# Kernel tuning notes

Measured on AMD Instinct MI355X. Metric: run time of the kernel, lower is better.

## Reference

```python
import jax, jax.numpy as jnp
import numpy as np

N = 100000       # nodes
D_IN = 256       # input feature dim
HID = 128        # hidden dim (GCN output)
D_OUT = 64       # SGCL output dim
NNZ = 1600000    # nnz of gcn adjacency
E = 500000       # directed edges (adj_e)
BIE = 1000000    # bidirectional edges (adj_n)


def setup_inputs() -> dict:
    key = jax.random.key(0)
    ks = jax.random.split(key, 13)
    X = jax.random.normal(ks[0], (N, D_IN), jnp.float32)
    # weight scales chosen so exp(logstd) stays well-conditioned (glorot-like)
    W_gcn = jax.random.normal(ks[1], (D_IN, HID), jnp.float32) * 0.05
    W_miu = jax.random.normal(ks[2], (2 * HID, D_OUT), jnp.float32) * 0.01
    W_sigma = jax.random.normal(ks[3], (2 * HID, D_OUT), jnp.float32) * 0.01
    gcn_values = jax.random.uniform(ks[4], (NNZ,), jnp.float32)
    bi_values = jax.random.uniform(ks[5], (BIE,), jnp.float32)
    noise_in = jax.random.normal(ks[6], (E, D_OUT), jnp.float32)
    noise_out = jax.random.normal(ks[7], (E, D_OUT), jnp.float32)
    noise_node = jax.random.normal(ks[8], (N, D_OUT), jnp.float32)
    gcn_indices = jax.random.randint(ks[9], (2, NNZ), 0, N)
    di_edges = jax.random.randint(ks[10], (2, E), 0, N)
    # ensure every node has at least one incident bi-edge (source side) so that
    # log(aggregated variance) is finite, as with a real symmetric adjacency
    bi_src = jnp.concatenate([jnp.arange(N), jax.random.randint(ks[11], (BIE - N,), 0, N)])
    bi_dst = jax.random.randint(ks[12], (BIE,), 0, N)
    bi_edges = jnp.stack([bi_src, bi_dst], axis=0)
    return {
        "X": X, "W_gcn": W_gcn, "W_miu": W_miu, "W_sigma": W_sigma,
        "gcn_values": gcn_values, "bi_values": bi_values,
        "noise_in": noise_in, "noise_out": noise_out, "noise_node": noise_node,
        "gcn_indices": gcn_indices, "di_edges": di_edges, "bi_edges": bi_edges,
    }


def reference(X, W_gcn, W_miu, W_sigma, gcn_values, bi_values,
              noise_in, noise_out, noise_node, gcn_indices, di_edges, bi_edges):
    n = X.shape[0]
    hid = W_gcn.shape[1]
    # ---- GraphConvSparse with identity activation: adj @ (X @ W) ----
    xw = X @ W_gcn                                     # [N, HID]
    msgs = gcn_values[:, None] * xw[gcn_indices[1]]    # [NNZ, HID]
    hidden = jax.ops.segment_sum(msgs, gcn_indices[0], num_segments=n)
    # split weights: concat([h_a, h_b]) @ W == h_a @ W_top + h_b @ W_bot
    Wm_t, Wm_b = W_miu[:hid], W_miu[hid:]
    Ws_t, Ws_b = W_sigma[:hid], W_sigma[hid:]
    # ---- edge embedding (directed edges) ----
    h_src = hidden[di_edges[0]]                        # [E, HID]
    h_dst = hidden[di_edges[1]]                        # [E, HID]
    miu_in = h_src @ Wm_t + h_dst @ Wm_b               # [E, D_OUT]
    miu_out = h_dst @ Wm_t + h_src @ Wm_b
    logstd_in = h_src @ Ws_t + h_dst @ Ws_b
    logstd_out = h_dst @ Ws_t + h_src @ Ws_b
    edge_in = noise_in * jnp.exp(logstd_in) + miu_in
    edge_out = noise_out * jnp.exp(logstd_out) + miu_out
    # ---- node embedding (bidirectional edges, weighted scatter-aggregate) ----
    b0 = hidden[bi_edges[0]]                           # [BIE, HID]
    b1 = hidden[bi_edges[1]]
    bi_miu = b0 @ Wm_t + b1 @ Wm_b                     # [BIE, D_OUT]
    bi_logstd = b0 @ Ws_t + b1 @ Ws_b
    node_miu = jax.ops.segment_sum(bi_values[:, None] * bi_miu, bi_edges[0], num_segments=n)
    node_var = jax.ops.segment_sum((bi_values ** 2)[:, None] * jnp.exp(bi_logstd), bi_edges[0], num_segments=n)
    node_logstd = 0.5 * jnp.log(node_var)
    node_embed = noise_node * jnp.exp(node_logstd) + node_miu
    return (node_embed, edge_in, edge_out)
```

## Files before the change

### kernel.cpp

```cpp
#include <hip/hip_runtime.h>

typedef unsigned short u16t;
typedef unsigned int   u32t;
typedef unsigned long long u64t;

#define NNODE 100000
#define DIN   256
#define HIDN  128
#define DOUTN 64
#define NNZE  1600000
#define EDIR  500000
#define EBI   1000000
#define G64   1563
#define NBIN  782
#define CH3   4096
#define K3G   391
#define K3B   245
#define CAPG  2432
#define CAPB  1536
#define EBLK  15625

typedef __attribute__((ext_vector_type(8))) short bf16x8;
typedef __attribute__((ext_vector_type(4))) float f32x4;
typedef __attribute__((ext_vector_type(4))) float f4v;

__device__ __forceinline__ u16t f2bf(float f){
  u32t u = __float_as_uint(f);
  u += 0x7FFFu + ((u>>16)&1u);
  return (u16t)(u>>16);
}
__device__ __forceinline__ float2 up2(u32t w){
  return make_float2(__uint_as_float(w<<16), __uint_as_float(w&0xFFFF0000u));
}

__global__ __launch_bounds__(256) void prep_kernel(const float* __restrict__ Wg,
                                                   const float* __restrict__ Wm,
                                                   const float* __restrict__ Wsg,
                                                   u16t* __restrict__ Wg_pre,
                                                   u16t* __restrict__ Wc_pre){
  int idx = blockIdx.x*256 + threadIdx.x;
  int e = idx & 7, l = (idx>>3) & 63, f = (idx>>9) & 63, sel = idx>>15;
  int k_in = ((e>>2)<<4) + ((l>>4)<<2) + (e&3);
  if(sel == 0){
    int ks = f>>3, nf = f&7;
    int k = ks*32 + k_in, n = nf*16 + (l&15);
    Wg_pre[idx] = f2bf(Wg[(size_t)k*HIDN + n]);
  } else {
    int ks = f>>4, nf = f&15;
    int k = ks*32 + k_in, c = nf*16 + (l&15);
    int half = c>>7, ci = c&127;
    const float* src = (ci&1) ? Wsg : Wm;
    Wc_pre[idx - 32768] = f2bf(src[(size_t)(half*128 + k)*DOUTN + (ci>>1)]);
  }
}

__global__ __launch_bounds__(256) void coarse_hist_kernel(const int* __restrict__ gi,
                                                          const int* __restrict__ be,
                                                          u32t* __restrict__ gcnt_c,
                                                          u32t* __restrict__ bcnt_c){
  __shared__ u32t h[1024];
  int blk = blockIdx.x, t = threadIdx.x;
  const int* keys; u32t* outc; int E, e0;
  if(blk < K3G){ keys=gi; outc=gcnt_c; E=NNZE; e0=blk*CH3; }
  else         { keys=be; outc=bcnt_c; E=EBI;  e0=(blk-K3G)*CH3; }
  for(int i=t;i<1024;i+=256) h[i]=0;
  __syncthreads();
  for(int i=t;i<CH3;i+=256){
    int e=e0+i;
    if(e<E) atomicAdd(&h[(u32t)keys[e]>>7], 1u);
  }
  __syncthreads();
  for(int b=t;b<1024;b+=256){
    u32t c=h[b];
    if(c) atomicAdd(&outc[b], c);
  }
}

__global__ __launch_bounds__(256) void scan_coarse_kernel(u32t* __restrict__ gcnt_c,
                                                          u32t* __restrict__ gcoff,
                                                          u32t* __restrict__ gcur_,
                                                          u32t* __restrict__ bcnt_c,
                                                          u32t* __restrict__ bcoff,
                                                          u32t* __restrict__ bcur_){
  __shared__ u32t part[256];
  u32t *cnt, *coff, *cur;
  if(blockIdx.x==0){ cnt=gcnt_c; coff=gcoff; cur=gcur_; }
  else             { cnt=bcnt_c; coff=bcoff; cur=bcur_; }
  int t = threadIdx.x;
  u32t ch[4], s=0;
  #pragma unroll
  for(int j=0;j<4;j++){ int idx=t*4+j; ch[j] = (idx<NBIN)? cnt[idx] : 0u; s+=ch[j]; }
  part[t]=s; __syncthreads();
  for(int off=1;off<256;off<<=1){
    u32t x=(t>=off)?part[t-off]:0u;
    __syncthreads();
    part[t]+=x;
    __syncthreads();
  }
  u32t run=(t==0)?0u:part[t-1];
  #pragma unroll
  for(int j=0;j<4;j++){
    int idx=t*4+j;
    if(idx<NBIN){ coff[idx]=run; cur[idx]=run; run+=ch[j]; }
  }
  if(t==255) coff[NBIN]=part[255];
}

__global__ __launch_bounds__(256) void part_kernel(const int* __restrict__ gi,
                                                   const float* __restrict__ gv,
                                                   const int* __restrict__ be,
                                                   const float* __restrict__ bv,
                                                   u32t* __restrict__ gcur_,
                                                   u64t* __restrict__ gbuck,
                                                   u32t* __restrict__ bcur_,
                                                   u64t* __restrict__ bbuck){
  __shared__ u32t hist[1024];
  __shared__ u32t scn[1024];
  __shared__ u32t part[256];
  __shared__ u32t base[1024];
  __shared__ u64t ebuf[CH3];
  __shared__ u16t binsArr[CH3];
  int blk = blockIdx.x, t = threadIdx.x;
  const int *keys, *pay; const float* val; u32t* cursor; u64t* buck; int E, e0;
  if(blk < K3G){ keys=gi; pay=gi+NNZE; val=gv; cursor=gcur_; buck=gbuck; E=NNZE; e0=blk*CH3; }
  else         { keys=be; pay=be+EBI;  val=bv; cursor=bcur_; buck=bbuck; E=EBI;  e0=(blk-K3G)*CH3; }
  for(int i=t;i<1024;i+=256) hist[i]=0;
  __syncthreads();
  for(int i=t;i<CH3;i+=256){
    int e=e0+i;
    if(e<E) atomicAdd(&hist[(u32t)keys[e]>>7], 1u);
  }
  __syncthreads();
  u32t ch[4], s=0;
  #pragma unroll
  for(int j=0;j<4;j++){ ch[j]=hist[t*4+j]; s+=ch[j]; }
  part[t]=s; __syncthreads();
  for(int off=1;off<256;off<<=1){
    u32t x=(t>=off)?part[t-off]:0u;
    __syncthreads();
    part[t]+=x;
    __syncthreads();
  }
  u32t run=(t==0)?0u:part[t-1];
  #pragma unroll
  for(int j=0;j<4;j++){ scn[t*4+j]=run; run+=ch[j]; }
  __syncthreads();
  for(int i=t;i<1024;i+=256) hist[i]=scn[i];
  __syncthreads();
  for(int i=t;i<CH3;i+=256){
    int e=e0+i;
    if(e<E){
      int k = keys[e];
      u32t b = (u32t)k>>7;
      u32t p = atomicAdd(&hist[b],1u);
      u64t ent = (u64t)((u32t)pay[e] | (((u32t)k&127u)<<20)) | ((u64t)__float_as_uint(val[e])<<32);
      ebuf[p]=ent; binsArr[p]=(u16t)b;
    }
  }
  __syncthreads();
  for(int b=t;b<1024;b+=256){
    u32t c = hist[b]-scn[b];
    base[b] = c ? atomicAdd(&cursor[b], c) : 0u;
  }
  __syncthreads();
  int totalValid = part[255];
  for(int i=t;i<totalValid;i+=256){
    u32t b = binsArr[i];
    buck[ (size_t)base[b] + (u32t)i - scn[b] ] = ebuf[i];
  }
}

__global__ __launch_bounds__(256) void gemm1_kernel(const float* __restrict__ X,
                                                    const u16t* __restrict__ Wg_pre,
                                                    u16t* __restrict__ xwb){
  __shared__ __align__(16) u16t Xs[64*256];
  const int t = threadIdx.x, l = t & 63, w = t >> 6;
  const int row0 = blockIdx.x * 64;
  for(int i=0;i<16;i++){
    int m = w*16 + i;
    int mg = min(row0 + m, NNODE-1);
    f4v f = __builtin_nontemporal_load((const f4v*)&X[(size_t)mg*DIN + l*4]);
    u32t lo = (u32t)f2bf(f[0]) | ((u32t)f2bf(f[1])<<16);
    u32t hi = (u32t)f2bf(f[2]) | ((u32t)f2bf(f[3])<<16);
    u32t* p = (u32t*)&Xs[m*256 + ((l ^ (m&15))<<2)];
    p[0] = lo; p[1] = hi;
  }
  __syncthreads();
  f32x4 acc[8];
  #pragma unroll
  for(int nf=0;nf<8;nf++) acc[nf] = (f32x4)(0.f);
  const int lm = l & 15, l4 = l >> 4;
  const int mrow = w*16 + lm;
  #pragma unroll 1
  for(int ks=0; ks<8; ks++){
    int kg = ks*8 + l4;
    union { uint2 u2[2]; bf16x8 v; } a;
    a.u2[0] = *(const uint2*)&Xs[mrow*256 + ((kg     ^ lm)<<2)];
    a.u2[1] = *(const uint2*)&Xs[mrow*256 + (((kg+4) ^ lm)<<2)];
    #pragma unroll
    for(int nf=0;nf<8;nf++){
      union { uint4 u4; bf16x8 v; } b;
      b.u4 = *(const uint4*)&Wg_pre[(size_t)((ks*8+nf)*64 + l)*8];
      acc[nf] = __builtin_amdgcn_mfma_f32_16x16x32_bf16(a.v, b.v, acc[nf], 0, 0, 0);
    }
  }
  #pragma unroll
  for(int r=0;r<4;r++){
    int gr = row0 + w*16 + l4*4 + r;
    if(gr < NNODE){
      #pragma unroll
      for(int nf=0;nf<8;nf++)
        xwb[(size_t)gr*HIDN + nf*16 + lm] = f2bf(acc[nf][r]);
    }
  }
}

__global__ __launch_bounds__(256) void gcn_gather2_kernel(const u16t* __restrict__ xwb,
                                                          const u64t* __restrict__ gbuck,
                                                          const u32t* __restrict__ gcoff,
                                                          u32t* __restrict__ hiddenw){
  __shared__ u64t ebuf[CAPG];
  __shared__ u32t hist[128], offs[129], cur[128], sc[128];
  int bin = blockIdx.x, t = threadIdx.x;
  u32t base = gcoff[bin], cnt = gcoff[bin+1] - base;
  if(t<128) hist[t]=0;
  __syncthreads();
  for(u32t i=t;i<cnt;i+=256)
    atomicAdd(&hist[(u32t)(gbuck[base+i]>>20)&127u], 1u);
  __syncthreads();
  if(t<128) sc[t]=hist[t];
  __syncthreads();
  for(int off=1;off<128;off<<=1){
    u32t x=(t>=off&&t<128)?sc[t-off]:0u;
    __syncthreads();
    if(t<128) sc[t]+=x;
    __syncthreads();
  }
  if(t<128){ offs[t+1]=sc[t]; cur[t]=sc[t]-hist[t]; if(t==0) offs[0]=0u; }
  __syncthreads();
  for(u32t i=t;i<cnt;i+=256){
    u64t e = gbuck[base+i];
    u32t p = atomicAdd(&cur[(u32t)(e>>20)&127u], 1u);
    ebuf[p]=e;
  }
  __syncthreads();
  int w=t>>6, l=t&63;
  const u32t* xww=(const u32t*)xwb;
  for(int idx=w; idx<128; idx+=4){
    int n = bin*128 + idx;
    if(n >= NNODE) continue;
    u32t s0=offs[idx], cnt2=offs[idx+1]-s0;
    float acc0=0.f, acc1=0.f;
    u32t nbr=(cnt2+3)&~3u;
    for(u32t j=0;j<nbr;j+=4){
      float2 xs[4]; float vs[4];
      #pragma unroll
      for(int q=0;q<4;q++){
        u32t jj=j+q;
        u64t e=(jj<cnt2)? ebuf[s0+jj] : 0ULL;
        vs[q]=__uint_as_float((u32t)(e>>32));
        xs[q]=up2(xww[(size_t)(e&0x1FFFFu)*64 + l]);
      }
      #pragma unroll
      for(int q=0;q<4;q++){ acc0+=vs[q]*xs[q].x; acc1+=vs[q]*xs[q].y; }
    }
    hiddenw[(size_t)n*64 + l] = (u32t)f2bf(acc0) | ((u32t)f2bf(acc1)<<16);
  }
}

__global__ __launch_bounds__(256) void gemm2_kernel(u32t* __restrict__ hiddenw,
                                                    const u16t* __restrict__ Wc_pre,
                                                    u16t* __restrict__ DSTw){
  __shared__ __align__(16) u16t Hs[64*128];
  const int t = threadIdx.x, l = t & 63, w = t >> 6;
  const int row0 = blockIdx.x * 64;
  for(int i=0;i<16;i++){
    int m = w*16 + i;
    int mg = min(row0 + m, NNODE-1);
    u32t v = hiddenw[(size_t)mg*64 + l];
    *(u32t*)&Hs[m*128 + (((l>>1) ^ (m&15))<<2) + ((l&1)<<1)] = v;
  }
  __syncthreads();
  f32x4 acc[16];
  #pragma unroll
  for(int nf=0;nf<16;nf++) acc[nf] = (f32x4)(0.f);
  const int lm = l & 15, l4 = l >> 4;
  const int mrow = w*16 + lm;
  #pragma unroll 1
  for(int ks=0; ks<4; ks++){
    int kg = ks*8 + l4;
    union { uint2 u2[2]; bf16x8 v; } a;
    a.u2[0] = *(const uint2*)&Hs[mrow*128 + ((kg     ^ lm)<<2)];
    a.u2[1] = *(const uint2*)&Hs[mrow*128 + (((kg+4) ^ lm)<<2)];
    #pragma unroll
    for(int nf=0;nf<16;nf++){
      union { uint4 u4; bf16x8 v; } b;
      b.u4 = *(const uint4*)&Wc_pre[(size_t)((ks*16+nf)*64 + l)*8];
      acc[nf] = __builtin_amdgcn_mfma_f32_16x16x32_bf16(a.v, b.v, acc[nf], 0, 0, 0);
    }
  }
  u16t* SRCw = (u16t*)hiddenw;
  #pragma unroll
  for(int r=0;r<4;r++){
    int gr = row0 + w*16 + l4*4 + r;
    if(gr < NNODE){
      #pragma unroll
      for(int nf=0;nf<8;nf++)
        SRCw[(size_t)gr*HIDN + nf*16 + lm] = f2bf(acc[nf][r]);
      #pragma unroll
      for(int nf=8;nf<16;nf++)
        DSTw[(size_t)gr*HIDN + (nf-8)*16 + lm] = f2bf(acc[nf][r]);
    }
  }
}

__global__ __launch_bounds__(256) void edgebi2_kernel(const u16t* __restrict__ SRCb,
                                                      const u16t* __restrict__ DSTb,
                                                      const int*  __restrict__ ed,
                                                      const float* __restrict__ nin,
                                                      const float* __restrict__ nout,
                                                      float* __restrict__ ein,
                                                      float* __restrict__ eout,
                                                      const u64t* __restrict__ bbuck,
                                                      const u32t* __restrict__ bcoff,
                                                      const float* __restrict__ nn,
                                                      float* __restrict__ outp){
  __shared__ u64t ebuf[CAPB];
  __shared__ u32t hist[128], offs[129], cur[128], sc[128];
  const int t = threadIdx.x;
  const u32t* Sw = (const u32t*)SRCb;
  const u32t* Dw = (const u32t*)DSTb;
  if(blockIdx.x >= NBIN){
    const int e0 = ((int)(blockIdx.x - NBIN)*4 + (t>>6))*8;
    const int l = t & 63;
    int s[8], d[8];
    #pragma unroll
    for(int q=0;q<8;q++){ s[q] = ed[e0+q]; d[q] = ed[EDIR+e0+q]; }
    float2 Ss[8], Ds[8], Sd[8], Dd[8];
    float ni[8], no[8];
    #pragma unroll
    for(int q=0;q<8;q++){
      Ss[q] = up2(Sw[(size_t)s[q]*64 + l]);
      Ds[q] = up2(Dw[(size_t)s[q]*64 + l]);
      Sd[q] = up2(Sw[(size_t)d[q]*64 + l]);
      Dd[q] = up2(Dw[(size_t)d[q]*64 + l]);
      ni[q] = __builtin_nontemporal_load(&nin[(size_t)(e0+q)*DOUTN + l]);
      no[q] = __builtin_nontemporal_load(&nout[(size_t)(e0+q)*DOUTN + l]);
    }
    #pragma unroll
    for(int q=0;q<8;q++){
      size_t o = (size_t)(e0+q)*DOUTN + l;
      float miu_in  = Ss[q].x + Dd[q].x, ls_in  = Ss[q].y + Dd[q].y;
      float miu_out = Sd[q].x + Ds[q].x, ls_out = Sd[q].y + Ds[q].y;
      __builtin_nontemporal_store(ni[q] * __expf(ls_in)  + miu_in,  &ein[o]);
      __builtin_nontemporal_store(no[q] * __expf(ls_out) + miu_out, &eout[o]);
    }
    return;
  }
  int bin = blockIdx.x;
  u32t base = bcoff[bin], cnt = bcoff[bin+1] - base;
  if(t<128) hist[t]=0;
  __syncthreads();
  for(u32t i=t;i<cnt;i+=256)
    atomicAdd(&hist[(u32t)(bbuck[base+i]>>20)&127u], 1u);
  __syncthreads();
  if(t<128) sc[t]=hist[t];
  __syncthreads();
  for(int off=1;off<128;off<<=1){
    u32t x=(t>=off&&t<128)?sc[t-off]:0u;
    __syncthreads();
    if(t<128) sc[t]+=x;
    __syncthreads();
  }
  if(t<128){ offs[t+1]=sc[t]; cur[t]=sc[t]-hist[t]; if(t==0) offs[0]=0u; }
  __syncthreads();
  for(u32t i=t;i<cnt;i+=256){
    u64t e = bbuck[base+i];
    u32t p = atomicAdd(&cur[(u32t)(e>>20)&127u], 1u);
    ebuf[p]=e;
  }
  __syncthreads();
  int w=t>>6, l=t&63;
  for(int idx=w; idx<128; idx+=4){
    int n = bin*128 + idx;
    if(n >= NNODE) continue;
    float2 S = up2(Sw[(size_t)n*64 + l]);
    u32t s0=offs[idx], cnt2=offs[idx+1]-s0;
    float nmiu=0.f, nvar=0.f;
    u32t nbr=(cnt2+3)&~3u;
    for(u32t j=0;j<nbr;j+=4){
      float2 Dq[4]; float vs[4];
      #pragma unroll
      for(int q=0;q<4;q++){
        u32t jj=j+q;
        u64t e=(jj<cnt2)? ebuf[s0+jj] : 0ULL;
        vs[q]=__uint_as_float((u32t)(e>>32));
        Dq[q]=up2(Dw[(size_t)(e&0x1FFFFu)*64 + l]);
      }
      #pragma unroll
      for(int q=0;q<4;q++){
        nmiu += vs[q]*(S.x+Dq[q].x);
        nvar += vs[q]*vs[q]*__expf(S.y+Dq[q].y);
      }
    }
    size_t o = (size_t)n*DOUTN + l;
    float nd = __builtin_nontemporal_load(&nn[o]);
    __builtin_nontemporal_store(nd*sqrtf(nvar) + nmiu, &outp[o]);
  }
}

extern "C" void kernel_launch(void* const* d_in, const int* in_sizes, int n_in,
                              void* d_out, int out_size, void* d_ws, size_t ws_size,
                              hipStream_t stream){
  const float* X    = (const float*)d_in[0];
  const float* Wg   = (const float*)d_in[1];
  const float* Wm   = (const float*)d_in[2];
  const float* Wsg  = (const float*)d_in[3];
  const float* gv   = (const float*)d_in[4];
  const float* bv   = (const float*)d_in[5];
  const float* nin  = (const float*)d_in[6];
  const float* nout = (const float*)d_in[7];
  const float* nnod = (const float*)d_in[8];
  const int*  gi   = (const int*)d_in[9];
  const int*  ed   = (const int*)d_in[10];
  const int*  be   = (const int*)d_in[11];

  char* ws = (char*)d_ws;
  u64t*  gbuck   = (u64t*)ws;
  u16t*  xwb     = (u16t*)(ws + 12800000);
  u32t*  gcnt_c  = (u32t*)(ws + 38400000);
  u32t*  bcnt_c  = (u32t*)(ws + 38404096);
  u32t*  gcoff   = (u32t*)(ws + 38408192);
  u32t*  gcur_   = (u32t*)(ws + 38412288);
  u32t*  bcoff   = (u32t*)(ws + 38416384);
  u32t*  bcur_   = (u32t*)(ws + 38420480);
  u64t*  bbuck   = (u64t*)(ws + 40003168);
  u32t*  hiddenw = (u32t*)(ws + 51200000);
  u16t*  SRCw    = (u16t*)hiddenw;
  u16t*  DSTw    = (u16t*)ws;

  float* out  = (float*)d_out;
  float* ein  = out + (size_t)NNODE*DOUTN;
  float* eout = ein + (size_t)EDIR*DOUTN;
  u16t* Wg_pre = (u16t*)((char*)d_out + 25600000 - 131072);
  u16t* Wc_pre = Wg_pre + 32768;

  (void)hipMemsetAsync(gcnt_c, 0, 8192, stream);
  coarse_hist_kernel<<<K3G+K3B, 256, 0, stream>>>(gi, be, gcnt_c, bcnt_c);
  scan_coarse_kernel<<<2,       256, 0, stream>>>(gcnt_c, gcoff, gcur_, bcnt_c, bcoff, bcur_);
  part_kernel       <<<K3G+K3B, 256, 0, stream>>>(gi, gv, be, bv, gcur_, gbuck, bcur_, bbuck);
  prep_kernel       <<<256,     256, 0, stream>>>(Wg, Wm, Wsg, Wg_pre, Wc_pre);
  gemm1_kernel      <<<G64,     256, 0, stream>>>(X, Wg_pre, xwb);
  gcn_gather2_kernel<<<NBIN,    256, 0, stream>>>(xwb, gbuck, gcoff, hiddenw);
  gemm2_kernel      <<<G64,     256, 0, stream>>>(hiddenw, Wc_pre, DSTw);
  edgebi2_kernel    <<<NBIN+EBLK, 256, 0, stream>>>(SRCw, DSTw, ed, nin, nout,
                                                    ein, eout, bbuck, bcoff, nnod, out);
}
```

Baseline: 446.7 us.

## Merge weight prep into histogram kernel and partition into gemm1 launch

```diff
diff --git a/kernel.cpp b/kernel.cpp
--- a/kernel.cpp
+++ b/kernel.cpp
@@ -16,6 +16,7 @@
 #define CH3   4096
 #define K3G   391
 #define K3B   245
+#define KPART (K3G+K3B)
 #define CAPG  2432
 #define CAPB  1536
 #define EBLK  15625
@@ -33,33 +34,34 @@
   return make_float2(__uint_as_float(w<<16), __uint_as_float(w&0xFFFF0000u));
 }
 
-__global__ __launch_bounds__(256) void prep_kernel(const float* __restrict__ Wg,
-                                                   const float* __restrict__ Wm,
-                                                   const float* __restrict__ Wsg,
-                                                   u16t* __restrict__ Wg_pre,
-                                                   u16t* __restrict__ Wc_pre){
-  int idx = blockIdx.x*256 + threadIdx.x;
-  int e = idx & 7, l = (idx>>3) & 63, f = (idx>>9) & 63, sel = idx>>15;
-  int k_in = ((e>>2)<<4) + ((l>>4)<<2) + (e&3);
-  if(sel == 0){
-    int ks = f>>3, nf = f&7;
-    int k = ks*32 + k_in, n = nf*16 + (l&15);
-    Wg_pre[idx] = f2bf(Wg[(size_t)k*HIDN + n]);
-  } else {
-    int ks = f>>4, nf = f&15;
-    int k = ks*32 + k_in, c = nf*16 + (l&15);
-    int half = c>>7, ci = c&127;
-    const float* src = (ci&1) ? Wsg : Wm;
-    Wc_pre[idx - 32768] = f2bf(src[(size_t)(half*128 + k)*DOUTN + (ci>>1)]);
-  }
-}
-
-__global__ __launch_bounds__(256) void coarse_hist_kernel(const int* __restrict__ gi,
-                                                          const int* __restrict__ be,
-                                                          u32t* __restrict__ gcnt_c,
-                                                          u32t* __restrict__ bcnt_c){
+__global__ __launch_bounds__(256) void histprep_kernel(const int* __restrict__ gi,
+                                                       const int* __restrict__ be,
+                                                       u32t* __restrict__ gcnt_c,
+                                                       u32t* __restrict__ bcnt_c,
+                                                       const float* __restrict__ Wg,
+                                                       const float* __restrict__ Wm,
+                                                       const float* __restrict__ Wsg,
+                                                       u16t* __restrict__ Wg_pre,
+                                                       u16t* __restrict__ Wc_pre){
   __shared__ u32t h[1024];
   int blk = blockIdx.x, t = threadIdx.x;
+  if(blk >= KPART){
+    int idx = (blk-KPART)*256 + t;
+    int e = idx & 7, l = (idx>>3) & 63, f = (idx>>9) & 63, sel = idx>>15;
+    int k_in = ((e>>2)<<4) + ((l>>4)<<2) + (e&3);
+    if(sel == 0){
+      int ks = f>>3, nf = f&7;
+      int k = ks*32 + k_in, n = nf*16 + (l&15);
+      Wg_pre[idx] = f2bf(Wg[(size_t)k*HIDN + n]);
+    } else {
+      int ks = f>>4, nf = f&15;
+      int k = ks*32 + k_in, c = nf*16 + (l&15);
+      int half = c>>7, ci = c&127;
+      const float* src = (ci&1) ? Wsg : Wm;
+      Wc_pre[idx - 32768] = f2bf(src[(size_t)(half*128 + k)*DOUTN + (ci>>1)]);
+    }
+    return;
+  }
   const int* keys; u32t* outc; int E, e0;
   if(blk < K3G){ keys=gi; outc=gcnt_c; E=NNZE; e0=blk*CH3; }
   else         { keys=be; outc=bcnt_c; E=EBI;  e0=(blk-K3G)*CH3; }
@@ -106,21 +108,68 @@
   if(t==255) coff[NBIN]=part[255];
 }
 
-__global__ __launch_bounds__(256) void part_kernel(const int* __restrict__ gi,
-                                                   const float* __restrict__ gv,
-                                                   const int* __restrict__ be,
-                                                   const float* __restrict__ bv,
-                                                   u32t* __restrict__ gcur_,
-                                                   u64t* __restrict__ gbuck,
-                                                   u32t* __restrict__ bcur_,
-                                                   u64t* __restrict__ bbuck){
-  __shared__ u32t hist[1024];
-  __shared__ u32t scn[1024];
-  __shared__ u32t part[256];
-  __shared__ u32t base[1024];
-  __shared__ u64t ebuf[CH3];
-  __shared__ u16t binsArr[CH3];
-  int blk = blockIdx.x, t = threadIdx.x;
+__global__ __launch_bounds__(256) void partgemm1_kernel(const float* __restrict__ X,
+                                                        const u16t* __restrict__ Wg_pre,
+                                                        u16t* __restrict__ xwb,
+                                                        const int* __restrict__ gi,
+                                                        const float* __restrict__ gv,
+                                                        const int* __restrict__ be,
+                                                        const float* __restrict__ bv,
+                                                        u32t* __restrict__ gcur_,
+                                                        u64t* __restrict__ gbuck,
+                                                        u32t* __restrict__ bcur_,
+                                                        u64t* __restrict__ bbuck){
+  __shared__ __align__(16) char smem[50176];
+  const int t = threadIdx.x;
+  if(blockIdx.x < G64){
+    u16t* Xs = (u16t*)smem;
+    const int l = t & 63, w = t >> 6;
+    const int row0 = blockIdx.x * 64;
+    for(int i=0;i<16;i++){
+      int m = w*16 + i;
+      int mg = min(row0 + m, NNODE-1);
+      f4v f = __builtin_nontemporal_load((const f4v*)&X[(size_t)mg*DIN + l*4]);
+      u32t lo = (u32t)f2bf(f[0]) | ((u32t)f2bf(f[1])<<16);
+      u32t hi = (u32t)f2bf(f[2]) | ((u32t)f2bf(f[3])<<16);
+      u32t* p = (u32t*)&Xs[m*256 + ((l ^ (m&15))<<2)];
+      p[0] = lo; p[1] = hi;
+    }
+    __syncthreads();
+    f32x4 acc[8];
+    #pragma unroll
+    for(int nf=0;nf<8;nf++) acc[nf] = (f32x4)(0.f);
+    const int lm = l & 15, l4 = l >> 4;
+    const int mrow = w*16 + lm;
+    #pragma unroll 1
+    for(int ks=0; ks<8; ks++){
+      int kg = ks*8 + l4;
+      union { uint2 u2[2]; bf16x8 v; } a;
+      a.u2[0] = *(const uint2*)&Xs[mrow*256 + ((kg     ^ lm)<<2)];
+      a.u2[1] = *(const uint2*)&Xs[mrow*256 + (((kg+4) ^ lm)<<2)];
+      #pragma unroll
+      for(int nf=0;nf<8;nf++){
+        union { uint4 u4; bf16x8 v; } b;
+        b.u4 = *(const uint4*)&Wg_pre[(size_t)((ks*8+nf)*64 + l)*8];
+        acc[nf] = __builtin_amdgcn_mfma_f32_16x16x32_bf16(a.v, b.v, acc[nf], 0, 0, 0);
+      }
+    }
+    #pragma unroll
+    for(int r=0;r<4;r++){
+      int gr = row0 + w*16 + l4*4 + r;
+      if(gr < NNODE){
+        #pragma unroll
+        for(int nf=0;nf<8;nf++)
+          xwb[(size_t)gr*HIDN + nf*16 + lm] = f2bf(acc[nf][r]);
+      }
+    }
+    return;
+  }
+  u32t* hist = (u32t*)smem;
+  u32t* scn  = (u32t*)(smem+4096);
+  u32t* prt  = (u32t*)(smem+8192);
+  u64t* ebuf = (u64t*)(smem+9216);
+  u16t* bins = (u16t*)(smem+41984);
+  int blk = blockIdx.x - G64;
   const int *keys, *pay; const float* val; u32t* cursor; u64t* buck; int E, e0;
   if(blk < K3G){ keys=gi; pay=gi+NNZE; val=gv; cursor=gcur_; buck=gbuck; E=NNZE; e0=blk*CH3; }
   else         { keys=be; pay=be+EBI;  val=bv; cursor=bcur_; buck=bbuck; E=EBI;  e0=(blk-K3G)*CH3; }
@@ -134,14 +183,14 @@
   u32t ch[4], s=0;
   #pragma unroll
   for(int j=0;j<4;j++){ ch[j]=hist[t*4+j]; s+=ch[j]; }
-  part[t]=s; __syncthreads();
+  prt[t]=s; __syncthreads();
   for(int off=1;off<256;off<<=1){
-    u32t x=(t>=off)?part[t-off]:0u;
-    __syncthreads();
-    part[t]+=x;
-    __syncthreads();
-  }
-  u32t run=(t==0)?0u:part[t-1];
+    u32t x=(t>=off)?prt[t-off]:0u;
+    __syncthreads();
+    prt[t]+=x;
+    __syncthreads();
+  }
+  u32t run=(t==0)?0u:prt[t-1];
   #pragma unroll
   for(int j=0;j<4;j++){ scn[t*4+j]=run; run+=ch[j]; }
   __syncthreads();
@@ -154,64 +203,20 @@
       u32t b = (u32t)k>>7;
       u32t p = atomicAdd(&hist[b],1u);
       u64t ent = (u64t)((u32t)pay[e] | (((u32t)k&127u)<<20)) | ((u64t)__float_as_uint(val[e])<<32);
-      ebuf[p]=ent; binsArr[p]=(u16t)b;
+      ebuf[p]=ent; bins[p]=(u16t)b;
     }
   }
   __syncthreads();
   for(int b=t;b<1024;b+=256){
     u32t c = hist[b]-scn[b];
-    base[b] = c ? atomicAdd(&cursor[b], c) : 0u;
-  }
-  __syncthreads();
-  int totalValid = part[255];
+    u32t bs = c ? atomicAdd(&cursor[b], c) : 0u;
+    hist[b] = bs;
+  }
+  __syncthreads();
+  int totalValid = prt[255];
   for(int i=t;i<totalValid;i+=256){
-    u32t b = binsArr[i];
-    buck[ (size_t)base[b] + (u32t)i - scn[b] ] = ebuf[i];
-  }
-}
-
-__global__ __launch_bounds__(256) void gemm1_kernel(const float* __restrict__ X,
-                                                    const u16t* __restrict__ Wg_pre,
-                                                    u16t* __restrict__ xwb){
-  __shared__ __align__(16) u16t Xs[64*256];
-  const int t = threadIdx.x, l = t & 63, w = t >> 6;
-  const int row0 = blockIdx.x * 64;
-  for(int i=0;i<16;i++){
-    int m = w*16 + i;
-    int mg = min(row0 + m, NNODE-1);
-    f4v f = __builtin_nontemporal_load((const f4v*)&X[(size_t)mg*DIN + l*4]);
-    u32t lo = (u32t)f2bf(f[0]) | ((u32t)f2bf(f[1])<<16);
-    u32t hi = (u32t)f2bf(f[2]) | ((u32t)f2bf(f[3])<<16);
-    u32t* p = (u32t*)&Xs[m*256 + ((l ^ (m&15))<<2)];
-    p[0] = lo; p[1] = hi;
-  }
-  __syncthreads();
-  f32x4 acc[8];
-  #pragma unroll
-  for(int nf=0;nf<8;nf++) acc[nf] = (f32x4)(0.f);
-  const int lm = l & 15, l4 = l >> 4;
-  const int mrow = w*16 + lm;
-  #pragma unroll 1
-  for(int ks=0; ks<8; ks++){
-    int kg = ks*8 + l4;
-    union { uint2 u2[2]; bf16x8 v; } a;
-    a.u2[0] = *(const uint2*)&Xs[mrow*256 + ((kg     ^ lm)<<2)];
-    a.u2[1] = *(const uint2*)&Xs[mrow*256 + (((kg+4) ^ lm)<<2)];
-    #pragma unroll
-    for(int nf=0;nf<8;nf++){
-      union { uint4 u4; bf16x8 v; } b;
-      b.u4 = *(const uint4*)&Wg_pre[(size_t)((ks*8+nf)*64 + l)*8];
-      acc[nf] = __builtin_amdgcn_mfma_f32_16x16x32_bf16(a.v, b.v, acc[nf], 0, 0, 0);
-    }
-  }
-  #pragma unroll
-  for(int r=0;r<4;r++){
-    int gr = row0 + w*16 + l4*4 + r;
-    if(gr < NNODE){
-      #pragma unroll
-      for(int nf=0;nf<8;nf++)
-        xwb[(size_t)gr*HIDN + nf*16 + lm] = f2bf(acc[nf][r]);
-    }
+    u32t b = bins[i];
+    buck[ (size_t)hist[b] + (u32t)i - scn[b] ] = ebuf[i];
   }
 }
 
@@ -446,13 +451,13 @@
   u16t* Wc_pre = Wg_pre + 32768;
 
   (void)hipMemsetAsync(gcnt_c, 0, 8192, stream);
-  coarse_hist_kernel<<<K3G+K3B, 256, 0, stream>>>(gi, be, gcnt_c, bcnt_c);
-  scan_coarse_kernel<<<2,       256, 0, stream>>>(gcnt_c, gcoff, gcur_, bcnt_c, bcoff, bcur_);
-  part_kernel       <<<K3G+K3B, 256, 0, stream>>>(gi, gv, be, bv, gcur_, gbuck, bcur_, bbuck);
-  prep_kernel       <<<256,     256, 0, stream>>>(Wg, Wm, Wsg, Wg_pre, Wc_pre);
-  gemm1_kernel      <<<G64,     256, 0, stream>>>(X, Wg_pre, xwb);
-  gcn_gather2_kernel<<<NBIN,    256, 0, stream>>>(xwb, gbuck, gcoff, hiddenw);
-  gemm2_kernel      <<<G64,     256, 0, stream>>>(hiddenw, Wc_pre, DSTw);
+  histprep_kernel   <<<KPART+256, 256, 0, stream>>>(gi, be, gcnt_c, bcnt_c,
+                                                    Wg, Wm, Wsg, Wg_pre, Wc_pre);
+  scan_coarse_kernel<<<2,         256, 0, stream>>>(gcnt_c, gcoff, gcur_, bcnt_c, bcoff, bcur_);
+  partgemm1_kernel  <<<G64+KPART, 256, 0, stream>>>(X, Wg_pre, xwb,
+                                                    gi, gv, be, bv, gcur_, gbuck, bcur_, bbuck);
+  gcn_gather2_kernel<<<NBIN,      256, 0, stream>>>(xwb, gbuck, gcoff, hiddenw);
+  gemm2_kernel      <<<G64,       256, 0, stream>>>(hiddenw, Wc_pre, DSTw);
   edgebi2_kernel    <<<NBIN+EBLK, 256, 0, stream>>>(SRCw, DSTw, ed, nin, nout,
                                                     ein, eout, bbuck, bcoff, nnod, out);
 }
```

Measured after the change: 422.3 us. 1.06x faster.
